# Kernel optimization log

Hardware: AMD Instinct MI355X
Metric: run time of the kernel (lower is better)

Reference implementation:

```python
import jax, jax.numpy as jnp
import numpy as np

N = 30000      # num nodes
E = 600000     # num edges
D = 128        # feature dim (all layers)
R = 7          # num_relation
G = 16         # num graphs in batch
L = 3          # num layers (hidden_dims = [128,128,128])


def setup_inputs() -> dict:
    key = jax.random.key(0)
    ks = jax.random.split(key, 10)
    x = jax.random.normal(ks[0], (N, D), dtype=jnp.float32)
    node_in = jax.random.randint(ks[1], (E,), 0, N)
    node_out = jax.random.randint(ks[2], (E,), 0, N)
    relation = jax.random.randint(ks[3], (E,), 0, R)
    edge_weight = jax.random.uniform(ks[4], (E,), dtype=jnp.float32)
    node2graph = jnp.sort(jax.random.randint(ks[5], (N,), 0, G))
    # learned params: per-layer relational linear (R*D -> D) and self-loop linear (D -> D)
    Wr = jax.random.normal(ks[6], (L, R * D, D), dtype=jnp.float32) * 0.02
    br = jnp.zeros((L, D), dtype=jnp.float32)
    Wl = jax.random.normal(ks[7], (L, D, D), dtype=jnp.float32) * 0.02
    bl = jnp.zeros((L, D), dtype=jnp.float32)
    return dict(x=x, node_in=node_in, node_out=node_out, relation=relation,
                edge_weight=edge_weight, node2graph=node2graph,
                Wr=Wr, br=br, Wl=Wl, bl=bl)


def reference(x, node_in, node_out, relation, edge_weight, node2graph, Wr, br, Wl, bl):
    # relation-indexed destination segment: node_out * R + relation
    seg = node_out * R + relation            # (E,)
    ew = edge_weight[:, None]                # (E, 1)
    h = x
    for i in range(L):
        msg = h[node_in] * ew                                         # gather + weight, (E, D)
        upd = jax.ops.segment_sum(msg, seg, num_segments=N * R)       # scatter_add, (N*R, D)
        upd = upd.reshape(N, R * D)                                   # per-relation concat
        h = jax.nn.relu(upd @ Wr[i] + br[i] + h @ Wl[i] + bl[i])      # linear + self-loop + act
    node_feature = h                                                  # (N, D)
    graph_feature = jax.ops.segment_sum(node_feature, node2graph, num_segments=G)  # sum readout
    return graph_feature, node_feature
```

## Files before the change

### kernel.cpp

```cpp
#include <hip/hip_runtime.h>
#include <hip/hip_bf16.h>

#define NN 30000
#define NE 600000
#define DD 128
#define RR 7
#define GG 16
#define LL 3

#define NB64 ((NN + 63) / 64)
#define NPACK (LL * 1024 * DD)
#define NCVT  (NN * 32)

typedef short bf16x8 __attribute__((ext_vector_type(8)));
typedef float f32x4  __attribute__((ext_vector_type(4)));
typedef float f32x2  __attribute__((ext_vector_type(2)));


__device__ __forceinline__ unsigned short f2bf(float f) {
    unsigned u = __float_as_uint(f);
    unsigned r = (u + 0x7fffu + ((u >> 16) & 1u)) >> 16;
    return (unsigned short)r;
}
__device__ __forceinline__ ushort2 pk2bf(float a, float b) {
    __hip_bfloat162 t = __float22bfloat162_rn(make_float2(a, b));
    return *(ushort2*)&t;
}

__device__ __forceinline__ void gl_lds16(const void* g, void* l) {
    __builtin_amdgcn_global_load_lds(
        (const __attribute__((address_space(1))) void*)g,
        (__attribute__((address_space(3))) void*)l, 16, 0, 0);
}

__global__ __launch_bounds__(256) void pack_and_convert(
    const float* __restrict__ Wl,
    const float* __restrict__ Wr,
    unsigned short* __restrict__ Bw,
    const float* __restrict__ x,
    unsigned short* __restrict__ hb,
    int* __restrict__ bcnt,
    float* __restrict__ gf)
{
    int t = blockIdx.x * 256 + threadIdx.x;
    if (t < NPACK) {
        int l = t >> 17;
        int rem = t & 131071;
        int n = rem >> 7;
        int k_pos = rem & 127;
        int kp = k_pos & 63;
        int k = (k_pos & ~63) + (kp & 3) * 16 + (kp >> 2);
        float v;
        if (n < DD) {
            v = Wl[(size_t)l * DD * DD + k * DD + n];
        } else {
            int q = n - DD;
            v = Wr[(size_t)l * RR * DD * DD + (size_t)((q >> 7) * DD + k) * DD + (q & 127)];
        }
        Bw[t] = f2bf(v);
    } else if (t < NPACK + NCVT) {
        int i = t - NPACK;
        int row = i >> 5;
        int pg  = i & 31;
        int span = pg >> 4;
        int q = pg & 15;
        const float* xr = x + (size_t)row * DD + span * 64 + q;
        ushort2 a = pk2bf(xr[0],  xr[16]);
        ushort2 b = pk2bf(xr[32], xr[48]);
        ((ushort4*)hb)[i] = make_ushort4(a.x, a.y, b.x, b.y);
    } else {
        int i = t - NPACK - NCVT;
        if (i < NB64 * 16) bcnt[i] = 0;
        else {
            i -= NB64 * 16;
            if (i < GG * DD) gf[i] = 0.f;
        }
    }
}

__global__ __launch_bounds__(256) void bucket_hist(
    const int* __restrict__ node_out, int* __restrict__ bcnt, int E)
{
    int e = blockIdx.x * 256 + threadIdx.x;
    if (e < E) atomicAdd(&bcnt[(node_out[e] >> 6) * 16], 1);
}

__global__ __launch_bounds__(512) void bucket_scan(
    const int* __restrict__ bcnt, int* __restrict__ bstart,
    int* __restrict__ bcur, int nb)
{
    __shared__ int s[512];
    int t = threadIdx.x;
    int v = (t < nb) ? bcnt[t * 16] : 0;
    s[t] = v;
    __syncthreads();
#pragma unroll
    for (int off = 1; off < 512; off <<= 1) {
        int u = (t >= off) ? s[t - off] : 0;
        __syncthreads();
        s[t] += u;
        __syncthreads();
    }
    if (t <= nb) {
        int excl = s[t] - v;
        bstart[t] = excl;
        if (t < nb) bcur[t * 16] = excl;
    }
}

__global__ __launch_bounds__(256) void bucket_scatter(
    const int* __restrict__ node_in,
    const int* __restrict__ node_out,
    const int* __restrict__ relation,
    const float* __restrict__ ew,
    int* __restrict__ bcur,
    int2* __restrict__ tmp,
    int E)
{
    int e = blockIdx.x * 256 + threadIdx.x;
    if (e >= E) return;
    int o = node_out[e];
    int pos = atomicAdd(&bcur[(o >> 6) * 16], 1);
    tmp[pos] = make_int2(((o & 63) << 18) | (node_in[e] << 3) | relation[e],
                         __float_as_int(ew[e]));
}

__global__ __launch_bounds__(256) void bucket_sort(
    const int2* __restrict__ tmp,
    const int* __restrict__ bstart,
    int2* __restrict__ meta,
    int* __restrict__ start,
    int N)
{
    __shared__ int hist[64];
    __shared__ int scan[64];
    __shared__ int cur[64];
    const int b = blockIdx.x;
    const int t = threadIdx.x;
    const int s0 = bstart[b];
    const int s1 = bstart[b + 1];

    if (t < 64) hist[t] = 0;
    __syncthreads();
    for (int i = s0 + t; i < s1; i += 256)
        atomicAdd(&hist[((unsigned)tmp[i].x) >> 18], 1);
    __syncthreads();

    int v = (t < 64) ? hist[t] : 0;
    if (t < 64) scan[t] = v;
    __syncthreads();
#pragma unroll
    for (int off = 1; off < 64; off <<= 1) {
        int u = (t < 64 && t >= off) ? scan[t - off] : 0;
        __syncthreads();
        if (t < 64) scan[t] += u;
        __syncthreads();
    }
    if (t < 64) {
        int excl = scan[t] - v;
        cur[t] = s0 + excl;
        int node = b * 64 + t;
        if (node <= N) start[node] = s0 + excl;
    }
    __syncthreads();

    for (int i = s0 + t; i < s1; i += 256) {
        int2 m = tmp[i];
        int j = ((unsigned)m.x) >> 18;
        int pos = atomicAdd(&cur[j], 1);
        int key = m.x & 0x3ffff;
        int in = key >> 3, rel = key & 7;
        meta[pos] = make_int2((in * RR + rel) << 7, m.y);
    }
}

__global__ __launch_bounds__(256) void gemm_mfma(
    const unsigned short* __restrict__ hb,
    const unsigned short* __restrict__ Bw,
    const float* __restrict__ br,
    const float* __restrict__ bl,
    unsigned short* __restrict__ haccb,
    unsigned char* __restrict__ Zb8,
    int N)
{
    __shared__ unsigned short As[64 * 128];
    __shared__ unsigned short Bs[256 * 128];

    const int tid  = threadIdx.x;
    const int wave = tid >> 6;
    const int lane = tid & 63;
    const int quad = lane >> 4;
    const int l16  = lane & 15;
    const int row0 = blockIdx.x * 64;
    const int col0 = blockIdx.y * 256;

    const int lr = lane >> 4;
    const int ls = lane & 15;

#pragma unroll
    for (int i = 0; i < 4; ++i) {
        int g = i * 4 + wave;
        int r = g * 4 + lr;
        int slot = ls ^ (r & 7);
        gl_lds16(hb + (size_t)(row0 + r) * 128 + slot * 8, As + g * 512);
    }
#pragma unroll
    for (int i = 0; i < 16; ++i) {
        int g = i * 4 + wave;
        int r = g * 4 + lr;
        int slot = ls ^ (r & 7);
        gl_lds16(Bw + (size_t)(col0 + r) * 128 + slot * 8, Bs + g * 512);
    }
    __syncthreads();

    f32x4 acc[4][4];
#pragma unroll
    for (int mt = 0; mt < 4; ++mt)
#pragma unroll
        for (int nt = 0; nt < 4; ++nt)
            acc[mt][nt] = (f32x4){0.f, 0.f, 0.f, 0.f};

    const unsigned short* As_l = As + l16 * 128;
    const unsigned short* Bs_l = Bs + (wave * 64 + l16) * 128;
    const int swz = l16 & 7;

#pragma unroll
    for (int kc = 0; kc < 4; ++kc) {
        int so = ((kc * 4 + quad) ^ swz) * 8;
        bf16x8 a0 = *(const bf16x8*)(As_l + 0 * 16 * 128 + so);
        bf16x8 a1 = *(const bf16x8*)(As_l + 1 * 16 * 128 + so);
        bf16x8 a2 = *(const bf16x8*)(As_l + 2 * 16 * 128 + so);
        bf16x8 a3 = *(const bf16x8*)(As_l + 3 * 16 * 128 + so);
        bf16x8 b0 = *(const bf16x8*)(Bs_l + 0 * 16 * 128 + so);
        bf16x8 b1 = *(const bf16x8*)(Bs_l + 1 * 16 * 128 + so);
        bf16x8 b2 = *(const bf16x8*)(Bs_l + 2 * 16 * 128 + so);
        bf16x8 b3 = *(const bf16x8*)(Bs_l + 3 * 16 * 128 + so);
#pragma unroll
        for (int mt = 0; mt < 4; ++mt) {
            bf16x8 a = (mt == 0) ? a0 : (mt == 1) ? a1 : (mt == 2) ? a2 : a3;
            acc[mt][0] = __builtin_amdgcn_mfma_f32_16x16x32_bf16(a, b0, acc[mt][0], 0, 0, 0);
            acc[mt][1] = __builtin_amdgcn_mfma_f32_16x16x32_bf16(a, b1, acc[mt][1], 0, 0, 0);
            acc[mt][2] = __builtin_amdgcn_mfma_f32_16x16x32_bf16(a, b2, acc[mt][2], 0, 0, 0);
            acc[mt][3] = __builtin_amdgcn_mfma_f32_16x16x32_bf16(a, b3, acc[mt][3], 0, 0, 0);
        }
    }

    if (col0 == 0 && wave < 2) {
        float bias[4];
#pragma unroll
        for (int nt = 0; nt < 4; ++nt) {
            int c = wave * 64 + nt * 16 + l16;
            bias[nt] = br[c] + bl[c];
        }
#pragma unroll
        for (int mt = 0; mt < 4; ++mt) {
#pragma unroll
            for (int reg = 0; reg < 4; ++reg) {
                int row = row0 + mt * 16 + quad * 4 + reg;
                if (row < N) {
                    ushort2 p01 = pk2bf(acc[mt][0][reg] + bias[0],
                                        acc[mt][1][reg] + bias[1]);
                    ushort2 p23 = pk2bf(acc[mt][2][reg] + bias[2],
                                        acc[mt][3][reg] + bias[3]);
                    *(ushort4*)(haccb + (size_t)row * 128 + wave * 64 + l16 * 4) =
                        make_ushort4(p01.x, p01.y, p23.x, p23.y);
                }
            }
        }
    } else {
        const int zpos = col0 + wave * 64 - 128;
#pragma unroll
        for (int mt = 0; mt < 4; ++mt) {
#pragma unroll
            for (int reg = 0; reg < 4; ++reg) {
                int row = row0 + mt * 16 + quad * 4 + reg;
                if (row < N) {
                    int u = __builtin_amdgcn_cvt_pk_fp8_f32(
                        acc[mt][0][reg], acc[mt][1][reg], 0, false);
                    u = __builtin_amdgcn_cvt_pk_fp8_f32(
                        acc[mt][2][reg], acc[mt][3][reg], u, true);
                    *(int*)(Zb8 + (size_t)row * (RR * DD) + zpos + l16 * 4) = u;
                }
            }
        }
    }
}

__global__ __launch_bounds__(256) void aggregate(
    const unsigned char* __restrict__ Zb8,
    const int* __restrict__ start,
    const int2* __restrict__ meta,
    const unsigned short* __restrict__ haccb,
    float* __restrict__ out_f32,
    unsigned short* __restrict__ out_bf16,
    int N)
{
    int wid = (blockIdx.x * 256 + threadIdx.x) >> 6;
    int lane = threadIdx.x & 63;
    if (wid >= N) return;

    const int grp  = lane >> 4;
    const int l16  = lane & 15;
    const int base = l16 * 8;

    int e0 = start[wid];
    int e1 = start[wid + 1];

    float acc[8];
#pragma unroll
    for (int k = 0; k < 8; ++k) acc[k] = 0.f;

#define FMA8(u, wt) do {                                                \
    f32x2 d0 = __builtin_amdgcn_cvt_pk_f32_fp8((u).x, false);           \
    f32x2 d1 = __builtin_amdgcn_cvt_pk_f32_fp8((u).x, true);            \
    f32x2 d2 = __builtin_amdgcn_cvt_pk_f32_fp8((u).y, false);           \
    f32x2 d3 = __builtin_amdgcn_cvt_pk_f32_fp8((u).y, true);            \
    acc[0] = fmaf((wt), d0[0], acc[0]);                                 \
    acc[1] = fmaf((wt), d0[1], acc[1]);                                 \
    acc[2] = fmaf((wt), d1[0], acc[2]);                                 \
    acc[3] = fmaf((wt), d1[1], acc[3]);                                 \
    acc[4] = fmaf((wt), d2[0], acc[4]);                                 \
    acc[5] = fmaf((wt), d2[1], acc[5]);                                 \
    acc[6] = fmaf((wt), d3[0], acc[6]);                                 \
    acc[7] = fmaf((wt), d3[1], acc[7]);                                 \
} while (0)

    int e = e0;
    for (; e + 8 <= e1; e += 8) {
        int2 m0 = meta[e + grp];
        int2 m1 = meta[e + 4 + grp];
        uint2 u0 = *(const uint2*)(Zb8 + (size_t)(unsigned)m0.x + base);
        uint2 u1 = *(const uint2*)(Zb8 + (size_t)(unsigned)m1.x + base);
        float w0 = __int_as_float(m0.y);
        float w1 = __int_as_float(m1.y);
        FMA8(u0, w0);
        FMA8(u1, w1);
    }
    for (; e + 4 <= e1; e += 4) {
        int2 m = meta[e + grp];
        uint2 u = *(const uint2*)(Zb8 + (size_t)(unsigned)m.x + base);
        float wt = __int_as_float(m.y);
        FMA8(u, wt);
    }
    if (e + grp < e1) {
        int2 m = meta[e + grp];
        uint2 u = *(const uint2*)(Zb8 + (size_t)(unsigned)m.x + base);
        float wt = __int_as_float(m.y);
        FMA8(u, wt);
    }
#undef FMA8

#pragma unroll
    for (int k = 0; k < 8; ++k) {
        acc[k] += __shfl_xor(acc[k], 16, 64);
        acc[k] += __shfl_xor(acc[k], 32, 64);
    }

    uint4 hb4 = *(const uint4*)(haccb + (size_t)wid * DD + base);
    float o[8];
    o[0] = fmaxf(__uint_as_float(hb4.x << 16)         + acc[0], 0.f);
    o[1] = fmaxf(__uint_as_float(hb4.x & 0xffff0000u) + acc[1], 0.f);
    o[2] = fmaxf(__uint_as_float(hb4.y << 16)         + acc[2], 0.f);
    o[3] = fmaxf(__uint_as_float(hb4.y & 0xffff0000u) + acc[3], 0.f);
    o[4] = fmaxf(__uint_as_float(hb4.z << 16)         + acc[4], 0.f);
    o[5] = fmaxf(__uint_as_float(hb4.z & 0xffff0000u) + acc[5], 0.f);
    o[6] = fmaxf(__uint_as_float(hb4.w << 16)         + acc[6], 0.f);
    o[7] = fmaxf(__uint_as_float(hb4.w & 0xffff0000u) + acc[7], 0.f);

    if (grp == 0) {
        if (out_bf16) {
            ushort2 p0 = pk2bf(o[0], o[1]);
            ushort2 p1 = pk2bf(o[2], o[3]);
            ushort2 p2 = pk2bf(o[4], o[5]);
            ushort2 p3 = pk2bf(o[6], o[7]);
            uint4 ub;
            ub.x = (unsigned)p0.x | ((unsigned)p0.y << 16);
            ub.y = (unsigned)p1.x | ((unsigned)p1.y << 16);
            ub.z = (unsigned)p2.x | ((unsigned)p2.y << 16);
            ub.w = (unsigned)p3.x | ((unsigned)p3.y << 16);
            *(uint4*)(out_bf16 + (size_t)wid * DD + base) = ub;
        }
        if (out_f32) {
            int cb = ((l16 >> 3) << 6) + ((l16 & 7) << 1);
            float* dst = out_f32 + (size_t)wid * DD;
#pragma unroll
            for (int j = 0; j < 4; ++j) {
                *(float2*)(dst + cb + j * 16) = make_float2(o[j], o[j + 4]);
            }
        }
    }
}

__global__ __launch_bounds__(256) void graph_sum(
    const float* __restrict__ nf,
    const int* __restrict__ n2g,
    float* __restrict__ gf,
    int N)
{
    int t = blockIdx.x * 256 + threadIdx.x;
    int chunk = t >> 5;
    int lane = t & 31;
    int n0 = chunk * 16;
    if (n0 >= N) return;
    int nend = n0 + 16; if (nend > N) nend = N;

    float4 acc = make_float4(0.f, 0.f, 0.f, 0.f);
    int curg = n2g[n0];
    for (int n = n0; n < nend; ++n) {
        int g = n2g[n];
        if (g != curg) {
            float* dst = gf + (size_t)curg * DD + lane * 4;
            atomicAdd(dst + 0, acc.x); atomicAdd(dst + 1, acc.y);
            atomicAdd(dst + 2, acc.z); atomicAdd(dst + 3, acc.w);
            acc = make_float4(0.f, 0.f, 0.f, 0.f);
            curg = g;
        }
        float4 v = *(const float4*)(nf + (size_t)n * DD + lane * 4);
        acc.x += v.x; acc.y += v.y; acc.z += v.z; acc.w += v.w;
    }
    float* dst = gf + (size_t)curg * DD + lane * 4;
    atomicAdd(dst + 0, acc.x); atomicAdd(dst + 1, acc.y);
    atomicAdd(dst + 2, acc.z); atomicAdd(dst + 3, acc.w);
}

extern "C" void kernel_launch(void* const* d_in, const int* in_sizes, int n_in,
                              void* d_out, int out_size, void* d_ws, size_t ws_size,
                              hipStream_t stream)
{
    const float* x        = (const float*)d_in[0];
    const int*   node_in  = (const int*)d_in[1];
    const int*   node_out = (const int*)d_in[2];
    const int*   relation = (const int*)d_in[3];
    const float* ew       = (const float*)d_in[4];
    const int*   n2g      = (const int*)d_in[5];
    const float* Wr       = (const float*)d_in[6];
    const float* br       = (const float*)d_in[7];
    const float* Wl       = (const float*)d_in[8];
    const float* bl       = (const float*)d_in[9];

    float* out = (float*)d_out;
    float* gf = out;
    float* nf = out + GG * DD;

    char* w = (char*)d_ws;
    unsigned char*  Zb8  = (unsigned char*)w;  w += (size_t)NN * RR * DD;
    unsigned short* haccb= (unsigned short*)w; w += (size_t)NN * DD * 2;
    unsigned short* hbA  = (unsigned short*)w; w += (size_t)NN * DD * 2;
    unsigned short* hbB  = (unsigned short*)w; w += (size_t)NN * DD * 2;
    unsigned short* Bw   = (unsigned short*)w; w += (size_t)LL * 1024 * DD * 2;
    int2*  meta   = (int2*)w;                  w += (size_t)NE * 8;
    int2*  tmp    = (int2*)w;                  w += (size_t)NE * 8;
    int*   start  = (int*)w;                   w += (size_t)(NN + 1) * 4 + 60;
    int*   bcnt   = (int*)w;                   w += (size_t)NB64 * 16 * 4 + 64;
    int*   bcur   = (int*)w;                   w += (size_t)NB64 * 16 * 4 + 64;
    int*   bstart = (int*)w;                   w += (size_t)(NB64 + 1) * 4 + 60;

    const int N = NN, E = NE;

    int ptot = NPACK + NCVT + NB64 * 16 + GG * DD;
    pack_and_convert<<<(ptot + 255) / 256, 256, 0, stream>>>(
        Wl, Wr, Bw, x, hbA, bcnt, gf);

    bucket_hist<<<(E + 255) / 256, 256, 0, stream>>>(node_out, bcnt, E);
    bucket_scan<<<1, 512, 0, stream>>>(bcnt, bstart, bcur, NB64);
    bucket_scatter<<<(E + 255) / 256, 256, 0, stream>>>(
        node_in, node_out, relation, ew, bcur, tmp, E);
    bucket_sort<<<NB64, 256, 0, stream>>>(tmp, bstart, meta, start, N);

    dim3 ggrid((N + 63) / 64, 4);
    unsigned short* hin = hbA;
    unsigned short* hnext = hbB;
    for (int l = 0; l < LL; ++l) {
        const float* br_l = br + (size_t)l * DD;
        const float* bl_l = bl + (size_t)l * DD;
        const unsigned short* Bw_l = Bw + (size_t)l * 1024 * DD;

        gemm_mfma<<<ggrid, 256, 0, stream>>>(hin, Bw_l, br_l, bl_l, haccb, Zb8, N);

        bool last = (l == LL - 1);
        aggregate<<<(N * 64 + 255) / 256, 256, 0, stream>>>(
            Zb8, start, meta, haccb,
            last ? nf : (float*)nullptr,
            last ? (unsigned short*)nullptr : hnext, N);

        unsigned short* t = hin; hin = hnext; hnext = t;
    }

    int chunks = (N + 15) / 16;
    graph_sum<<<(chunks * 32 + 255) / 256, 256, 0, stream>>>(nf, n2g, gf, N);
}
```

Baseline: 288.4 us.

## Restructure GEMM to loop over weight chunks per row tile with smaller LDS

The GEMM now launches one block per 64-row tile instead of a 2D grid of 4 column groups, so the A tile is loaded once and reused across all 1024 output columns. The weight matrix is streamed through LDS in eight 128-column chunks, which halves the B buffer and should raise occupancy. The cost is a sequential chunk loop with two barriers per chunk and no overlap between B loads and MFMA work, plus fewer blocks in the grid.

```diff
diff --git a/kernel.cpp b/kernel.cpp
--- a/kernel.cpp
+++ b/kernel.cpp
@@ -21,6 +21,9 @@
     unsigned u = __float_as_uint(f);
     unsigned r = (u + 0x7fffu + ((u >> 16) & 1u)) >> 16;
     return (unsigned short)r;
+}
+__device__ __forceinline__ float bf2f(unsigned short b) {
+    return __uint_as_float(((unsigned)b) << 16);
 }
 __device__ __forceinline__ ushort2 pk2bf(float a, float b) {
     __hip_bfloat162 t = __float22bfloat162_rn(make_float2(a, b));
@@ -184,7 +187,7 @@
     int N)
 {
     __shared__ unsigned short As[64 * 128];
-    __shared__ unsigned short Bs[256 * 128];
+    __shared__ unsigned short Bs[128 * 128];
 
     const int tid  = threadIdx.x;
     const int wave = tid >> 6;
@@ -192,7 +195,6 @@
     const int quad = lane >> 4;
     const int l16  = lane & 15;
     const int row0 = blockIdx.x * 64;
-    const int col0 = blockIdx.y * 256;
 
     const int lr = lane >> 4;
     const int ls = lane & 15;
@@ -205,81 +207,78 @@
         gl_lds16(hb + (size_t)(row0 + r) * 128 + slot * 8, As + g * 512);
     }
 #pragma unroll
-    for (int i = 0; i < 16; ++i) {
+    for (int i = 0; i < 8; ++i) {
         int g = i * 4 + wave;
         int r = g * 4 + lr;
         int slot = ls ^ (r & 7);
-        gl_lds16(Bw + (size_t)(col0 + r) * 128 + slot * 8, Bs + g * 512);
-    }
-    __syncthreads();
-
-    f32x4 acc[4][4];
-#pragma unroll
-    for (int mt = 0; mt < 4; ++mt)
-#pragma unroll
-        for (int nt = 0; nt < 4; ++nt)
-            acc[mt][nt] = (f32x4){0.f, 0.f, 0.f, 0.f};
-
-    const unsigned short* As_l = As + l16 * 128;
-    const unsigned short* Bs_l = Bs + (wave * 64 + l16) * 128;
+        gl_lds16(Bw + (size_t)r * 128 + slot * 8, Bs + g * 512);
+    }
+
+    const unsigned short* As_w = As + (wave * 16 + l16) * 128;
+    const unsigned short* Bs_l = Bs + l16 * 128;
     const int swz = l16 & 7;
 
-#pragma unroll
-    for (int kc = 0; kc < 4; ++kc) {
-        int so = ((kc * 4 + quad) ^ swz) * 8;
-        bf16x8 a0 = *(const bf16x8*)(As_l + 0 * 16 * 128 + so);
-        bf16x8 a1 = *(const bf16x8*)(As_l + 1 * 16 * 128 + so);
-        bf16x8 a2 = *(const bf16x8*)(As_l + 2 * 16 * 128 + so);
-        bf16x8 a3 = *(const bf16x8*)(As_l + 3 * 16 * 128 + so);
-        bf16x8 b0 = *(const bf16x8*)(Bs_l + 0 * 16 * 128 + so);
-        bf16x8 b1 = *(const bf16x8*)(Bs_l + 1 * 16 * 128 + so);
-        bf16x8 b2 = *(const bf16x8*)(Bs_l + 2 * 16 * 128 + so);
-        bf16x8 b3 = *(const bf16x8*)(Bs_l + 3 * 16 * 128 + so);
-#pragma unroll
-        for (int mt = 0; mt < 4; ++mt) {
-            bf16x8 a = (mt == 0) ? a0 : (mt == 1) ? a1 : (mt == 2) ? a2 : a3;
-            acc[mt][0] = __builtin_amdgcn_mfma_f32_16x16x32_bf16(a, b0, acc[mt][0], 0, 0, 0);
-            acc[mt][1] = __builtin_amdgcn_mfma_f32_16x16x32_bf16(a, b1, acc[mt][1], 0, 0, 0);
-            acc[mt][2] = __builtin_amdgcn_mfma_f32_16x16x32_bf16(a, b2, acc[mt][2], 0, 0, 0);
-            acc[mt][3] = __builtin_amdgcn_mfma_f32_16x16x32_bf16(a, b3, acc[mt][3], 0, 0, 0);
-        }
-    }
-
-    if (col0 == 0 && wave < 2) {
-        float bias[4];
-#pragma unroll
-        for (int nt = 0; nt < 4; ++nt) {
-            int c = wave * 64 + nt * 16 + l16;
-            bias[nt] = br[c] + bl[c];
-        }
-#pragma unroll
-        for (int mt = 0; mt < 4; ++mt) {
+    for (int ch = 0; ch < 8; ++ch) {
+        if (ch > 0) {
+            __syncthreads();
+            const unsigned short* Bsrc = Bw + (size_t)ch * 16384;
+#pragma unroll
+            for (int i = 0; i < 8; ++i) {
+                int g = i * 4 + wave;
+                int r = g * 4 + lr;
+                int slot = ls ^ (r & 7);
+                gl_lds16(Bsrc + (size_t)r * 128 + slot * 8, Bs + g * 512);
+            }
+        }
+        __syncthreads();
+
+        f32x4 acc[8];
+#pragma unroll
+        for (int nt = 0; nt < 8; ++nt) acc[nt] = (f32x4){0.f, 0.f, 0.f, 0.f};
+
+#pragma unroll
+        for (int kc = 0; kc < 4; ++kc) {
+            int so = ((kc * 4 + quad) ^ swz) * 8;
+            bf16x8 a = *(const bf16x8*)(As_w + so);
+#pragma unroll
+            for (int nt = 0; nt < 8; ++nt) {
+                bf16x8 b = *(const bf16x8*)(Bs_l + nt * 16 * 128 + so);
+                acc[nt] = __builtin_amdgcn_mfma_f32_16x16x32_bf16(a, b, acc[nt], 0, 0, 0);
+            }
+        }
+
+        if (ch == 0) {
+            float bias[8];
+#pragma unroll
+            for (int nt = 0; nt < 8; ++nt) {
+                int c = nt * 16 + l16;
+                bias[nt] = br[c] + bl[c];
+            }
 #pragma unroll
             for (int reg = 0; reg < 4; ++reg) {
-                int row = row0 + mt * 16 + quad * 4 + reg;
+                int row = row0 + wave * 16 + quad * 4 + reg;
                 if (row < N) {
-                    ushort2 p01 = pk2bf(acc[mt][0][reg] + bias[0],
-                                        acc[mt][1][reg] + bias[1]);
-                    ushort2 p23 = pk2bf(acc[mt][2][reg] + bias[2],
-                                        acc[mt][3][reg] + bias[3]);
-                    *(ushort4*)(haccb + (size_t)row * 128 + wave * 64 + l16 * 4) =
-                        make_ushort4(p01.x, p01.y, p23.x, p23.y);
+                    ushort2 p01 = pk2bf(acc[0][reg] + bias[0], acc[1][reg] + bias[1]);
+                    ushort2 p23 = pk2bf(acc[2][reg] + bias[2], acc[3][reg] + bias[3]);
+                    ushort2 p45 = pk2bf(acc[4][reg] + bias[4], acc[5][reg] + bias[5]);
+                    ushort2 p67 = pk2bf(acc[6][reg] + bias[6], acc[7][reg] + bias[7]);
+                    unsigned short* dst = haccb + (size_t)row * 128 + l16 * 4;
+                    *(ushort4*)(dst)      = make_ushort4(p01.x, p01.y, p23.x, p23.y);
+                    *(ushort4*)(dst + 64) = make_ushort4(p45.x, p45.y, p67.x, p67.y);
                 }
             }
-        }
-    } else {
-        const int zpos = col0 + wave * 64 - 128;
-#pragma unroll
-        for (int mt = 0; mt < 4; ++mt) {
+        } else {
 #pragma unroll
             for (int reg = 0; reg < 4; ++reg) {
-                int row = row0 + mt * 16 + quad * 4 + reg;
+                int row = row0 + wave * 16 + quad * 4 + reg;
                 if (row < N) {
-                    int u = __builtin_amdgcn_cvt_pk_fp8_f32(
-                        acc[mt][0][reg], acc[mt][1][reg], 0, false);
-                    u = __builtin_amdgcn_cvt_pk_fp8_f32(
-                        acc[mt][2][reg], acc[mt][3][reg], u, true);
-                    *(int*)(Zb8 + (size_t)row * (RR * DD) + zpos + l16 * 4) = u;
+                    int u0 = __builtin_amdgcn_cvt_pk_fp8_f32(acc[0][reg], acc[1][reg], 0, false);
+                    u0 = __builtin_amdgcn_cvt_pk_fp8_f32(acc[2][reg], acc[3][reg], u0, true);
+                    int u1 = __builtin_amdgcn_cvt_pk_fp8_f32(acc[4][reg], acc[5][reg], 0, false);
+                    u1 = __builtin_amdgcn_cvt_pk_fp8_f32(acc[6][reg], acc[7][reg], u1, true);
+                    unsigned char* dst = Zb8 + (size_t)row * (RR * DD) + (ch - 1) * 128 + l16 * 4;
+                    *(int*)(dst)      = u0;
+                    *(int*)(dst + 64) = u1;
                 }
             }
         }
@@ -467,7 +466,6 @@
         node_in, node_out, relation, ew, bcur, tmp, E);
     bucket_sort<<<NB64, 256, 0, stream>>>(tmp, bstart, meta, start, N);
 
-    dim3 ggrid((N + 63) / 64, 4);
     unsigned short* hin = hbA;
     unsigned short* hnext = hbB;
     for (int l = 0; l < LL; ++l) {
@@ -475,7 +473,8 @@
         const float* bl_l = bl + (size_t)l * DD;
         const unsigned short* Bw_l = Bw + (size_t)l * 1024 * DD;
 
-        gemm_mfma<<<ggrid, 256, 0, stream>>>(hin, Bw_l, br_l, bl_l, haccb, Zb8, N);
+        gemm_mfma<<<(N + 63) / 64, 256, 0, stream>>>(
+            hin, Bw_l, br_l, bl_l, haccb, Zb8, N);
 
         bool last = (l == LL - 1);
         aggregate<<<(N * 64 + 255) / 256, 256, 0, stream>>>(
```

Result: no change. 293.1 us (+1.6%).

## Fuse bucket histogram into pack kernel and graph readout into final aggregate

Applied to the files above, without the earlier changes.

Folds the edge-bucket histogram into the pack/convert kernel, using a memset to zero the counters, and drops the separate graph_sum kernel. The last-layer aggregate now also sums node features per graph: an LDS reduction handles the block's leading graph and direct global atomics handle other graphs. This removes two kernel launches and one re-read of the node features, at the cost of extra atomics and barriers in the aggregate. The early `wid >= N` return was removed, so this relies on N being exactly divisible into full blocks (30000*64/256 is an integer) to avoid out-of-bounds reads.

```diff
diff --git a/kernel.cpp b/kernel.cpp
--- a/kernel.cpp
+++ b/kernel.cpp
@@ -22,6 +22,9 @@
     unsigned r = (u + 0x7fffu + ((u >> 16) & 1u)) >> 16;
     return (unsigned short)r;
 }
+__device__ __forceinline__ float bf2f(unsigned short b) {
+    return __uint_as_float(((unsigned)b) << 16);
+}
 __device__ __forceinline__ ushort2 pk2bf(float a, float b) {
     __hip_bfloat162 t = __float22bfloat162_rn(make_float2(a, b));
     return *(ushort2*)&t;
@@ -39,8 +42,10 @@
     unsigned short* __restrict__ Bw,
     const float* __restrict__ x,
     unsigned short* __restrict__ hb,
+    float* __restrict__ gf,
+    const int* __restrict__ node_out,
     int* __restrict__ bcnt,
-    float* __restrict__ gf)
+    int E)
 {
     int t = blockIdx.x * 256 + threadIdx.x;
     if (t < NPACK) {
@@ -68,21 +73,12 @@
         ushort2 a = pk2bf(xr[0],  xr[16]);
         ushort2 b = pk2bf(xr[32], xr[48]);
         ((ushort4*)hb)[i] = make_ushort4(a.x, a.y, b.x, b.y);
+    } else if (t < NPACK + NCVT + GG * DD) {
+        gf[t - NPACK - NCVT] = 0.f;
     } else {
-        int i = t - NPACK - NCVT;
-        if (i < NB64 * 16) bcnt[i] = 0;
-        else {
-            i -= NB64 * 16;
-            if (i < GG * DD) gf[i] = 0.f;
-        }
-    }
-}
-
-__global__ __launch_bounds__(256) void bucket_hist(
-    const int* __restrict__ node_out, int* __restrict__ bcnt, int E)
-{
-    int e = blockIdx.x * 256 + threadIdx.x;
-    if (e < E) atomicAdd(&bcnt[(node_out[e] >> 6) * 16], 1);
+        int e = t - NPACK - NCVT - GG * DD;
+        if (e < E) atomicAdd(&bcnt[(node_out[e] >> 6) * 16], 1);
+    }
 }
 
 __global__ __launch_bounds__(512) void bucket_scan(
@@ -291,13 +287,18 @@
     const int* __restrict__ start,
     const int2* __restrict__ meta,
     const unsigned short* __restrict__ haccb,
+    const int* __restrict__ n2g,
+    float* __restrict__ gf,
     float* __restrict__ out_f32,
     unsigned short* __restrict__ out_bf16,
     int N)
 {
-    int wid = (blockIdx.x * 256 + threadIdx.x) >> 6;
-    int lane = threadIdx.x & 63;
-    if (wid >= N) return;
+    __shared__ float gacc[128];
+    __shared__ int g0s;
+
+    const int tid  = threadIdx.x;
+    int wid = (blockIdx.x * 256 + tid) >> 6;
+    int lane = tid & 63;
 
     const int grp  = lane >> 4;
     const int l16  = lane & 15;
@@ -367,8 +368,8 @@
     o[6] = fmaxf(__uint_as_float(hb4.w << 16)         + acc[6], 0.f);
     o[7] = fmaxf(__uint_as_float(hb4.w & 0xffff0000u) + acc[7], 0.f);
 
-    if (grp == 0) {
-        if (out_bf16) {
+    if (out_bf16) {
+        if (grp == 0) {
             ushort2 p0 = pk2bf(o[0], o[1]);
             ushort2 p1 = pk2bf(o[2], o[3]);
             ushort2 p2 = pk2bf(o[4], o[5]);
@@ -380,47 +381,36 @@
             ub.w = (unsigned)p3.x | ((unsigned)p3.y << 16);
             *(uint4*)(out_bf16 + (size_t)wid * DD + base) = ub;
         }
-        if (out_f32) {
-            int cb = ((l16 >> 3) << 6) + ((l16 & 7) << 1);
+    }
+    if (out_f32) {
+        int cb = ((l16 >> 3) << 6) + ((l16 & 7) << 1);
+        if (grp == 0) {
             float* dst = out_f32 + (size_t)wid * DD;
 #pragma unroll
             for (int j = 0; j < 4; ++j) {
                 *(float2*)(dst + cb + j * 16) = make_float2(o[j], o[j + 4]);
             }
         }
-    }
-}
-
-__global__ __launch_bounds__(256) void graph_sum(
-    const float* __restrict__ nf,
-    const int* __restrict__ n2g,
-    float* __restrict__ gf,
-    int N)
-{
-    int t = blockIdx.x * 256 + threadIdx.x;
-    int chunk = t >> 5;
-    int lane = t & 31;
-    int n0 = chunk * 16;
-    if (n0 >= N) return;
-    int nend = n0 + 16; if (nend > N) nend = N;
-
-    float4 acc = make_float4(0.f, 0.f, 0.f, 0.f);
-    int curg = n2g[n0];
-    for (int n = n0; n < nend; ++n) {
-        int g = n2g[n];
-        if (g != curg) {
-            float* dst = gf + (size_t)curg * DD + lane * 4;
-            atomicAdd(dst + 0, acc.x); atomicAdd(dst + 1, acc.y);
-            atomicAdd(dst + 2, acc.z); atomicAdd(dst + 3, acc.w);
-            acc = make_float4(0.f, 0.f, 0.f, 0.f);
-            curg = g;
-        }
-        float4 v = *(const float4*)(nf + (size_t)n * DD + lane * 4);
-        acc.x += v.x; acc.y += v.y; acc.z += v.z; acc.w += v.w;
-    }
-    float* dst = gf + (size_t)curg * DD + lane * 4;
-    atomicAdd(dst + 0, acc.x); atomicAdd(dst + 1, acc.y);
-    atomicAdd(dst + 2, acc.z); atomicAdd(dst + 3, acc.w);
+        int g = n2g[wid];
+        if (tid == 0) g0s = g;
+        for (int i = tid; i < 128; i += 256) gacc[i] = 0.f;
+        __syncthreads();
+        int g0 = g0s;
+        if (grp == 0) {
+            if (g == g0) {
+#pragma unroll
+                for (int j = 0; j < 8; ++j)
+                    atomicAdd(&gacc[cb + (j & 3) * 16 + (j >> 2)], o[j]);
+            } else {
+                float* dst = gf + (size_t)g * DD;
+#pragma unroll
+                for (int j = 0; j < 8; ++j)
+                    atomicAdd(dst + cb + (j & 3) * 16 + (j >> 2), o[j]);
+            }
+        }
+        __syncthreads();
+        if (tid < 128) atomicAdd(gf + (size_t)g0 * DD + tid, gacc[tid]);
+    }
 }
 
 extern "C" void kernel_launch(void* const* d_in, const int* in_sizes, int n_in,
@@ -457,11 +447,11 @@
 
     const int N = NN, E = NE;
 
-    int ptot = NPACK + NCVT + NB64 * 16 + GG * DD;
+    hipMemsetAsync(bcnt, 0, (size_t)NB64 * 16 * sizeof(int), stream);
+    int ptot = NPACK + NCVT + GG * DD + E;
     pack_and_convert<<<(ptot + 255) / 256, 256, 0, stream>>>(
-        Wl, Wr, Bw, x, hbA, bcnt, gf);
-
-    bucket_hist<<<(E + 255) / 256, 256, 0, stream>>>(node_out, bcnt, E);
+        Wl, Wr, Bw, x, hbA, gf, node_out, bcnt, E);
+
     bucket_scan<<<1, 512, 0, stream>>>(bcnt, bstart, bcur, NB64);
     bucket_scatter<<<(E + 255) / 256, 256, 0, stream>>>(
         node_in, node_out, relation, ew, bcur, tmp, E);
@@ -479,13 +469,11 @@
 
         bool last = (l == LL - 1);
         aggregate<<<(N * 64 + 255) / 256, 256, 0, stream>>>(
-            Zb8, start, meta, haccb,
+            Zb8, start, meta, haccb, n2g,
+            last ? gf : (float*)nullptr,
             last ? nf : (float*)nullptr,
             last ? (unsigned short*)nullptr : hnext, N);
 
         unsigned short* t = hin; hin = hnext; hnext = t;
     }
-
-    int chunks = (N + 15) / 16;
-    graph_sum<<<(chunks * 32 + 255) / 256, 256, 0, stream>>>(nf, n2g, gf, N);
-}
+}
```

Result: slower. 301.3 us (+4.5%).
